# Kernel tuning notes

Measured on AMD Instinct MI355X. Metric: run time of the kernel, lower is better.

## Reference

```python
import jax, jax.numpy as jnp
import numpy as np

BINS = 8
EPS = 1e-12  # torch F.normalize default eps


def _pairwise_scores(matf):
    # torch: input1[a,b]=matf[b]; transpose(0,1)->matf[a]; transpose(-2,-1)->matf[a]^T [M,F]
    # matmul with input1[a,b]=matf[b] -> scores[a,b] = matf[a]^T @ matf[b], shape [M,M]
    bs, F, M = matf.shape
    s = jnp.einsum('afm,bfn->abmn', matf, matf)  # [bs, bs, M, M]
    return s.reshape(bs * bs, M * M)


def _histc_rows(x, bins):
    # torch.histc semantics with min=max=0: range = [row.min(), row.max()],
    # values == max land in the last bin.
    mn = jnp.min(x, axis=1, keepdims=True)
    mx = jnp.max(x, axis=1, keepdims=True)
    denom = jnp.where(mx > mn, mx - mn, jnp.ones_like(mx))
    idx = jnp.clip(jnp.floor((x - mn) / denom * bins).astype(jnp.int32), 0, bins - 1)
    nbs = x.shape[0]
    flat = (idx + (jnp.arange(nbs, dtype=jnp.int32) * bins)[:, None]).ravel()
    h = jnp.zeros(nbs * bins, dtype=x.dtype).at[flat].add(1.0)
    return h.reshape(nbs, bins)


def _l2_normalize(h):
    n = jnp.linalg.norm(h, axis=-1, keepdims=True)
    return h / jnp.maximum(n, EPS)


def setup_inputs() -> dict:
    key = jax.random.key(0)
    k1, k2 = jax.random.split(key)
    bs, F, M = 64, 256, 128
    matf1 = jax.random.normal(k1, (bs, F, M), dtype=jnp.float32)
    matf2 = jax.random.normal(k2, (bs, F, M), dtype=jnp.float32)
    return {"matf1": matf1, "matf2": matf2}


def reference(matf1, matf2):
    # scores are .detach()ed in the original; stop_gradient for faithfulness
    scores1 = jax.lax.stop_gradient(_pairwise_scores(matf1))  # [nbs, M*M]
    scores2 = jax.lax.stop_gradient(_pairwise_scores(matf2))
    h1 = _l2_normalize(_histc_rows(scores1, BINS))  # [nbs, 8]
    h2 = _l2_normalize(_histc_rows(scores2, BINS))
    return jnp.concatenate([h1, h2], axis=-1)  # [nbs, 16]
```

## Files before the change

kernel.cpp:

```cpp
#include <hip/hip_runtime.h>
#include <math.h>

#define BS 64
#define F  256
#define M  128
#define MF (M * F)
#define NBP 1056

typedef unsigned short u16;
typedef _Float16 f16x8 __attribute__((ext_vector_type(8)));
typedef float    f32x16 __attribute__((ext_vector_type(16)));


__global__ __launch_bounds__(256) void convert_f16_kernel(
    const float* __restrict__ m1, const float* __restrict__ m2,
    u16* __restrict__ hT)
{
    __shared__ float tile[64 * M];
    const int mat = blockIdx.x >> 6;
    const int b   = blockIdx.x & 63;
    const int f0  = blockIdx.y * 64;
    const float* src = (mat == 0 ? m1 : m2) + (size_t)b * MF + (size_t)f0 * M;
    const int tid = threadIdx.x;

    const float4* g = (const float4*)src;
    float4* s = (float4*)tile;
    #pragma unroll
    for (int i = 0; i < 8; ++i)
        s[tid + i * 256] = g[tid + i * 256];
    __syncthreads();

    const size_t obase = ((size_t)(mat * BS + b) * 32 + (f0 >> 3)) * 1024;
    #pragma unroll
    for (int it = 0; it < 4; ++it) {
        const int idx = it * 256 + tid;
        const int f8l = idx >> 7;
        const int m   = idx & 127;
        u16 hh[8] __attribute__((aligned(16)));
        #pragma unroll
        for (int j = 0; j < 8; ++j) {
            const float x = tile[(f8l * 8 + j) * M + m];
            const _Float16 h = (_Float16)x;
            hh[j] = __builtin_bit_cast(u16, h);
        }
        *(uint4*)&hT[obase + (size_t)idx * 8] = *(const uint4*)hh;
    }
}

__device__ __forceinline__ void async16(const u16* g, u16* l) {
    __builtin_amdgcn_global_load_lds(
        (const __attribute__((address_space(1))) unsigned int*)g,
        (__attribute__((address_space(3))) unsigned int*)l, 16, 0, 0);
}

__global__ __launch_bounds__(256, 2) void gram_hist_mfma(
    const u16* __restrict__ hT, float* __restrict__ out)
{
    __shared__ u16 lds[2 * 12288];
    __shared__ float smin[4], smax[4];
    __shared__ int hist[2][8];

    const int tid  = threadIdx.x;
    const int lane = tid & 63;
    const int w    = tid >> 6;

    if (tid < 16) hist[tid >> 3][tid & 7] = 0;

    int p = blockIdx.x, a = 0;
    { int cnt = 32; while (p >= cnt) { p -= cnt; ++a; cnt = (64 - a + 1) >> 1; } }
    const int b1 = a + 2 * p;
    int b2 = b1 + 1;
    const bool b2valid = (b2 <= 63);
    if (!b2valid) b2 = b1;
    const int mat = blockIdx.y;

    const u16* Asrc  = hT + (size_t)(mat * BS + a)  * MF;
    const u16* B1src = hT + (size_t)(mat * BS + b1) * MF;
    const u16* B2src = hT + (size_t)(mat * BS + b2) * MF;

    auto stage = [&](int bufo, int k0) {
        const int koff = k0 * 128;
        #pragma unroll
        for (int g = 0; g < 6; ++g) {
            const int idx = (g & 1) * 256 + tid;
            const u16* s = (g < 2 ? Asrc : (g < 4 ? B1src : B2src)) + koff + idx * 8;
            async16(s, &lds[bufo + (g >> 1) * 4096 + idx * 8]);
        }
    };

    const int pp = w >> 1;
    const int c  = w & 1;
    const int l31   = lane & 31;
    const int lhalf = lane >> 5;

    f32x16 acc[4][2];
    #pragma unroll
    for (int ti = 0; ti < 4; ++ti)
        #pragma unroll
        for (int u = 0; u < 2; ++u)
            #pragma unroll
            for (int r = 0; r < 16; ++r) acc[ti][u][r] = 0.0f;

    stage(0, 0);
    __syncthreads();

    for (int it = 0; it < 8; ++it) {
        const int cur = (it & 1) * 12288;
        if (it < 7) stage(cur ^ 12288, (it + 1) * 32);

        #pragma unroll
        for (int kk = 0; kk < 2; ++kk) {
            const int kb = kk * 2 + lhalf;
            f16x8 af[4], bf[2];
            #pragma unroll
            for (int t = 0; t < 4; ++t)
                af[t] = *(const f16x8*)&lds[cur + (kb * 128 + t * 32 + l31) * 8];
            #pragma unroll
            for (int t = 0; t < 2; ++t)
                bf[t] = *(const f16x8*)&lds[cur + (1 + pp) * 4096 + (kb * 128 + c * 64 + t * 32 + l31) * 8];
            #pragma unroll
            for (int ti = 0; ti < 4; ++ti)
                #pragma unroll
                for (int u = 0; u < 2; ++u)
                    acc[ti][u] = __builtin_amdgcn_mfma_f32_32x32x16_f16(af[ti], bf[u], acc[ti][u], 0, 0, 0);
        }
        __syncthreads();
    }

    float vmin = acc[0][0][0], vmax = vmin;
    #pragma unroll
    for (int ti = 0; ti < 4; ++ti)
        #pragma unroll
        for (int u = 0; u < 2; ++u)
            #pragma unroll
            for (int r = 0; r < 16; ++r) {
                vmin = fminf(vmin, acc[ti][u][r]);
                vmax = fmaxf(vmax, acc[ti][u][r]);
            }
    #pragma unroll
    for (int off = 1; off < 64; off <<= 1) {
        vmin = fminf(vmin, __shfl_xor(vmin, off, 64));
        vmax = fmaxf(vmax, __shfl_xor(vmax, off, 64));
    }
    if (lane == 0) { smin[w] = vmin; smax[w] = vmax; }
    __syncthreads();
    const float pmn = fminf(smin[pp * 2], smin[pp * 2 + 1]);
    const float pmx = fmaxf(smax[pp * 2], smax[pp * 2 + 1]);
    const float denom = (pmx > pmn) ? (pmx - pmn) : 1.0f;
    const float scale = 8.0f / denom;
    const float bias  = -pmn * scale;

    unsigned w0 = 0, w1 = 0;
    #pragma unroll
    for (int ti = 0; ti < 4; ++ti)
        #pragma unroll
        for (int u = 0; u < 2; ++u)
            #pragma unroll
            for (int r = 0; r < 16; ++r) {
                const float t = fmaf(acc[ti][u][r], scale, bias);
                int k = (int)t;
                k = k > 7 ? 7 : k;
                const unsigned inc = 1u << ((k & 3) * 8);
                if (k < 4) w0 += inc; else w1 += inc;
            }
    unsigned e0 = (w0 & 0xFFu)         | (((w0 >> 8)  & 0xFFu) << 16);
    unsigned e1 = ((w0 >> 16) & 0xFFu) | (((w0 >> 24) & 0xFFu) << 16);
    unsigned e2 = (w1 & 0xFFu)         | (((w1 >> 8)  & 0xFFu) << 16);
    unsigned e3 = ((w1 >> 16) & 0xFFu) | (((w1 >> 24) & 0xFFu) << 16);
    #pragma unroll
    for (int off = 32; off > 0; off >>= 1) {
        e0 += __shfl_down(e0, off, 64);
        e1 += __shfl_down(e1, off, 64);
        e2 += __shfl_down(e2, off, 64);
        e3 += __shfl_down(e3, off, 64);
    }
    if (lane == 0) {
        atomicAdd(&hist[pp][0], (int)(e0 & 0xFFFFu)); atomicAdd(&hist[pp][1], (int)(e0 >> 16));
        atomicAdd(&hist[pp][2], (int)(e1 & 0xFFFFu)); atomicAdd(&hist[pp][3], (int)(e1 >> 16));
        atomicAdd(&hist[pp][4], (int)(e2 & 0xFFFFu)); atomicAdd(&hist[pp][5], (int)(e2 >> 16));
        atomicAdd(&hist[pp][6], (int)(e3 & 0xFFFFu)); atomicAdd(&hist[pp][7], (int)(e3 >> 16));
    }
    __syncthreads();

    const int B = (pp == 0) ? b1 : b2;
    const bool valid = (pp == 0) || b2valid;
    if (valid && c == 0 && lane < 8) {
        float ss = 0.0f;
        #pragma unroll
        for (int k = 0; k < 8; ++k) {
            const float cc = (float)hist[pp][k];
            ss += cc * cc;
        }
        const float nrm = fmaxf(sqrtf(ss), 1e-12f);
        const float v = (float)hist[pp][lane] / nrm;
        out[((size_t)a * BS + B) * 16 + mat * 8 + lane] = v;
        if (a != B)
            out[((size_t)B * BS + a) * 16 + mat * 8 + lane] = v;
    }
}

extern "C" void kernel_launch(void* const* d_in, const int* in_sizes, int n_in,
                              void* d_out, int out_size, void* d_ws, size_t ws_size,
                              hipStream_t stream) {
    const float* m1 = (const float*)d_in[0];
    const float* m2 = (const float*)d_in[1];
    float* out = (float*)d_out;

    u16* hT = (u16*)d_ws;

    convert_f16_kernel<<<dim3(128, 4), 256, 0, stream>>>(m1, m2, hT);
    gram_hist_mfma<<<dim3(NBP, 2), 256, 0, stream>>>(hT, out);
}
```

Baseline: 119.0 us.

## Fuse conversion and gram-histogram into one persistent cooperative kernel

Merges the fp16 conversion kernel and the MFMA gram/histogram kernel into a single cooperative launch of 512 persistent blocks. A grid-wide sync separates the conversion phase from the pair loop, and each block then strides over the 2112 pair jobs. The goal is to remove the second launch and the gap between kernels. In exchange it adds grid-sync cost and a fixed persistent grid that may balance work less well than a full launch. If the cooperative launch fails, it falls back to the original two kernels.

```diff
diff --git a/kernel.cpp b/kernel.cpp
--- a/kernel.cpp
+++ b/kernel.cpp
@@ -1,16 +1,210 @@
 #include <hip/hip_runtime.h>
+#include <hip/hip_cooperative_groups.h>
 #include <math.h>
+
+namespace cg = cooperative_groups;
 
 #define BS 64
 #define F  256
 #define M  128
 #define MF (M * F)
 #define NBP 1056
+#define NJOBS (2 * NBP)
+#define GRID 512
 
 typedef unsigned short u16;
 typedef _Float16 f16x8 __attribute__((ext_vector_type(8)));
 typedef float    f32x16 __attribute__((ext_vector_type(16)));
 
+__device__ __forceinline__ void async16(const u16* g, u16* l) {
+    __builtin_amdgcn_global_load_lds(
+        (const __attribute__((address_space(1))) unsigned int*)g,
+        (__attribute__((address_space(3))) unsigned int*)l, 16, 0, 0);
+}
+
+__global__ __launch_bounds__(256, 2) void fused_kernel(
+    const float* __restrict__ m1, const float* __restrict__ m2,
+    u16* __restrict__ hT, float* __restrict__ out)
+{
+    __shared__ u16 lds[2 * 12288];
+    __shared__ float smin[4], smax[4];
+    __shared__ int hist[2][8];
+
+    const int tid  = threadIdx.x;
+    const int lane = tid & 63;
+    const int w    = tid >> 6;
+
+    {
+        const int unit = blockIdx.x;
+        const int mat = unit >> 8;
+        const int b   = (unit >> 2) & 63;
+        const int f0  = (unit & 3) * 64;
+        const float* src = (mat == 0 ? m1 : m2) + (size_t)b * MF + (size_t)f0 * M;
+        float* tile = (float*)lds;
+
+        const float4* g = (const float4*)src;
+        float4* s = (float4*)tile;
+        #pragma unroll
+        for (int i = 0; i < 8; ++i)
+            s[tid + i * 256] = g[tid + i * 256];
+        __syncthreads();
+
+        const size_t obase = ((size_t)(mat * BS + b) * 32 + (f0 >> 3)) * 1024;
+        #pragma unroll
+        for (int it = 0; it < 4; ++it) {
+            const int idx = it * 256 + tid;
+            const int f8l = idx >> 7;
+            const int m   = idx & 127;
+            u16 hh[8] __attribute__((aligned(16)));
+            #pragma unroll
+            for (int j = 0; j < 8; ++j) {
+                const float x = tile[(f8l * 8 + j) * M + m];
+                const _Float16 h = (_Float16)x;
+                hh[j] = __builtin_bit_cast(u16, h);
+            }
+            *(uint4*)&hT[obase + (size_t)idx * 8] = *(const uint4*)hh;
+        }
+    }
+
+    cg::this_grid().sync();
+
+    for (int job = blockIdx.x; job < NJOBS; job += GRID) {
+        __syncthreads();
+        if (tid < 16) hist[tid >> 3][tid & 7] = 0;
+
+        const int mat = (job >= NBP) ? 1 : 0;
+        int p = job - mat * NBP, a = 0;
+        { int cnt = 32; while (p >= cnt) { p -= cnt; ++a; cnt = (64 - a + 1) >> 1; } }
+        const int b1 = a + 2 * p;
+        int b2 = b1 + 1;
+        const bool b2valid = (b2 <= 63);
+        if (!b2valid) b2 = b1;
+
+        const u16* Asrc  = hT + (size_t)(mat * BS + a)  * MF;
+        const u16* B1src = hT + (size_t)(mat * BS + b1) * MF;
+        const u16* B2src = hT + (size_t)(mat * BS + b2) * MF;
+
+        auto stage = [&](int bufo, int k0) {
+            const int koff = k0 * 128;
+            #pragma unroll
+            for (int g = 0; g < 6; ++g) {
+                const int idx = (g & 1) * 256 + tid;
+                const u16* s = (g < 2 ? Asrc : (g < 4 ? B1src : B2src)) + koff + idx * 8;
+                async16(s, &lds[bufo + (g >> 1) * 4096 + idx * 8]);
+            }
+        };
+
+        const int pp = w >> 1;
+        const int c  = w & 1;
+        const int l31   = lane & 31;
+        const int lhalf = lane >> 5;
+
+        f32x16 acc[4][2];
+        #pragma unroll
+        for (int ti = 0; ti < 4; ++ti)
+            #pragma unroll
+            for (int u = 0; u < 2; ++u)
+                #pragma unroll
+                for (int r = 0; r < 16; ++r) acc[ti][u][r] = 0.0f;
+
+        stage(0, 0);
+        __syncthreads();
+
+        for (int it = 0; it < 8; ++it) {
+            const int cur = (it & 1) * 12288;
+            if (it < 7) stage(cur ^ 12288, (it + 1) * 32);
+
+            #pragma unroll
+            for (int kk = 0; kk < 2; ++kk) {
+                const int kb = kk * 2 + lhalf;
+                f16x8 af[4], bf[2];
+                #pragma unroll
+                for (int t = 0; t < 4; ++t)
+                    af[t] = *(const f16x8*)&lds[cur + (kb * 128 + t * 32 + l31) * 8];
+                #pragma unroll
+                for (int t = 0; t < 2; ++t)
+                    bf[t] = *(const f16x8*)&lds[cur + (1 + pp) * 4096 + (kb * 128 + c * 64 + t * 32 + l31) * 8];
+                #pragma unroll
+                for (int ti = 0; ti < 4; ++ti)
+                    #pragma unroll
+                    for (int u = 0; u < 2; ++u)
+                        acc[ti][u] = __builtin_amdgcn_mfma_f32_32x32x16_f16(af[ti], bf[u], acc[ti][u], 0, 0, 0);
+            }
+            __syncthreads();
+        }
+
+        float vmin = acc[0][0][0], vmax = vmin;
+        #pragma unroll
+        for (int ti = 0; ti < 4; ++ti)
+            #pragma unroll
+            for (int u = 0; u < 2; ++u)
+                #pragma unroll
+                for (int r = 0; r < 16; ++r) {
+                    vmin = fminf(vmin, acc[ti][u][r]);
+                    vmax = fmaxf(vmax, acc[ti][u][r]);
+                }
+        #pragma unroll
+        for (int off = 1; off < 64; off <<= 1) {
+            vmin = fminf(vmin, __shfl_xor(vmin, off, 64));
+            vmax = fmaxf(vmax, __shfl_xor(vmax, off, 64));
+        }
+        if (lane == 0) { smin[w] = vmin; smax[w] = vmax; }
+        __syncthreads();
+        const float pmn = fminf(smin[pp * 2], smin[pp * 2 + 1]);
+        const float pmx = fmaxf(smax[pp * 2], smax[pp * 2 + 1]);
+        const float denom = (pmx > pmn) ? (pmx - pmn) : 1.0f;
+        const float scale = 8.0f / denom;
+        const float bias  = -pmn * scale;
+
+        unsigned w0 = 0, w1 = 0;
+        #pragma unroll
+        for (int ti = 0; ti < 4; ++ti)
+            #pragma unroll
+            for (int u = 0; u < 2; ++u)
+                #pragma unroll
+                for (int r = 0; r < 16; ++r) {
+                    const float t = fmaf(acc[ti][u][r], scale, bias);
+                    int k = (int)t;
+                    k = k > 7 ? 7 : k;
+                    const unsigned inc = 1u << ((k & 3) * 8);
+                    if (k < 4) w0 += inc; else w1 += inc;
+                }
+        unsigned e0 = (w0 & 0xFFu)         | (((w0 >> 8)  & 0xFFu) << 16);
+        unsigned e1 = ((w0 >> 16) & 0xFFu) | (((w0 >> 24) & 0xFFu) << 16);
+        unsigned e2 = (w1 & 0xFFu)         | (((w1 >> 8)  & 0xFFu) << 16);
+        unsigned e3 = ((w1 >> 16) & 0xFFu) | (((w1 >> 24) & 0xFFu) << 16);
+        #pragma unroll
+        for (int off = 32; off > 0; off >>= 1) {
+            e0 += __shfl_down(e0, off, 64);
+            e1 += __shfl_down(e1, off, 64);
+            e2 += __shfl_down(e2, off, 64);
+            e3 += __shfl_down(e3, off, 64);
+        }
+        if (lane == 0) {
+            atomicAdd(&hist[pp][0], (int)(e0 & 0xFFFFu)); atomicAdd(&hist[pp][1], (int)(e0 >> 16));
+            atomicAdd(&hist[pp][2], (int)(e1 & 0xFFFFu)); atomicAdd(&hist[pp][3], (int)(e1 >> 16));
+            atomicAdd(&hist[pp][4], (int)(e2 & 0xFFFFu)); atomicAdd(&hist[pp][5], (int)(e2 >> 16));
+            atomicAdd(&hist[pp][6], (int)(e3 & 0xFFFFu)); atomicAdd(&hist[pp][7], (int)(e3 >> 16));
+        }
+        __syncthreads();
+
+        const int B = (pp == 0) ? b1 : b2;
+        const bool valid = (pp == 0) || b2valid;
+        if (valid && c == 0 && lane < 8) {
+            float ss = 0.0f;
+            #pragma unroll
+            for (int k = 0; k < 8; ++k) {
+                const float cc = (float)hist[pp][k];
+                ss += cc * cc;
+            }
+            const float nrm = fmaxf(sqrtf(ss), 1e-12f);
+            const float v = (float)hist[pp][lane] / nrm;
+            out[((size_t)a * BS + B) * 16 + mat * 8 + lane] = v;
+            if (a != B)
+                out[((size_t)B * BS + a) * 16 + mat * 8 + lane] = v;
+        }
+    }
+}
 
 __global__ __launch_bounds__(256) void convert_f16_kernel(
     const float* __restrict__ m1, const float* __restrict__ m2,
@@ -47,12 +241,6 @@
     }
 }
 
-__device__ __forceinline__ void async16(const u16* g, u16* l) {
-    __builtin_amdgcn_global_load_lds(
-        (const __attribute__((address_space(1))) unsigned int*)g,
-        (__attribute__((address_space(3))) unsigned int*)l, 16, 0, 0);
-}
-
 __global__ __launch_bounds__(256, 2) void gram_hist_mfma(
     const u16* __restrict__ hT, float* __restrict__ out)
 {
@@ -208,6 +396,12 @@
 
     u16* hT = (u16*)d_ws;
 
-    convert_f16_kernel<<<dim3(128, 4), 256, 0, stream>>>(m1, m2, hT);
-    gram_hist_mfma<<<dim3(NBP, 2), 256, 0, stream>>>(hT, out);
+    void* args[] = { (void*)&m1, (void*)&m2, (void*)&hT, (void*)&out };
+    hipError_t err = hipLaunchCooperativeKernel(
+        (const void*)fused_kernel, dim3(GRID), dim3(256), args, 0, stream);
+
+    if (err != hipSuccess) {
+        convert_f16_kernel<<<dim3(128, 4), 256, 0, stream>>>(m1, m2, hT);
+        gram_hist_mfma<<<dim3(NBP, 2), 256, 0, stream>>>(hT, out);
+    }
 }
```

New measurement: 201.4 us. +69.2%, slower.
